# Kernel optimization log

Hardware: AMD Instinct MI355X
Metric: run time of the kernel (lower is better)

## Reference

```python
import jax, jax.numpy as jnp
import numpy as np
from jax import lax

IMG, P, C, D, H, L, B = 256, 16, 3, 768, 12, 8, 2
G = IMG // P            # 16
N = G * G               # 256 patches
FF = 2048               # hard-coded FFN hidden dim in ViTBlockWithCCAttention
DH = D // H
EPS = 1e-5


def setup_inputs() -> dict:
    key = jax.random.key(0)
    ks = jax.random.split(key, 24)
    s = 0.02
    rn = lambda k, shp: jax.random.normal(k, shp, jnp.float32) * s
    inp = {
        "x": jax.random.normal(ks[0], (B, C, IMG, IMG), jnp.float32),
        "patch_w": rn(ks[1], (D, C * P * P)),
        "patch_b": rn(ks[2], (D,)),
        "pos_embed": rn(ks[3], (1, N, D)),
        # per-layer stacked params (shared nn.MultiheadAttention per block)
        "in_proj_w": rn(ks[4], (L, 3 * D, D)),
        "in_proj_b": rn(ks[5], (L, 3 * D)),
        "out_w": rn(ks[6], (L, D, D)),
        "out_b": rn(ks[7], (L, D)),
        "ln1_g": jnp.ones((L, D), jnp.float32),
        "ln1_b": jnp.zeros((L, D), jnp.float32),
        "ln2_g": jnp.ones((L, D), jnp.float32),
        "ln2_b": jnp.zeros((L, D), jnp.float32),
        "ffn_w1": rn(ks[8], (L, FF, D)),
        "ffn_b1": rn(ks[9], (L, FF)),
        "ffn_w2": rn(ks[10], (L, D, FF)),
        "ffn_b2": rn(ks[11], (L, D)),
        "edge_w": rn(ks[12], (D, 1)),
        "edge_b": rn(ks[13], (D,)),
        "conv1_w": rn(ks[14], (256, D, 3, 3)),
        "conv1_b": rn(ks[15], (256,)),
        "conv2_w": rn(ks[16], (1, 256, 1, 1)),
        "conv2_b": rn(ks[17], (1,)),
    }
    return inp


def _ln(z, g, b):
    m = z.mean(-1, keepdims=True)
    v = ((z - m) ** 2).mean(-1, keepdims=True)
    return (z - m) / jnp.sqrt(v + EPS) * g + b


def _mha(z, wi, bi, wo, bo):
    # z: (M, S, D). Returns out (M,S,D) and head-averaged attn weights (M,S,S)
    M, S, _ = z.shape
    qkv = z @ wi.T + bi
    q, k, v = jnp.split(qkv, 3, axis=-1)
    sp = lambda t: t.reshape(M, S, H, DH).transpose(0, 2, 1, 3)  # (M,H,S,dh)
    q, k, v = sp(q), sp(k), sp(v)
    a = jax.nn.softmax(jnp.einsum('mhqd,mhkd->mhqk', q, k) / np.sqrt(DH).astype(np.float32), axis=-1)
    o = jnp.einsum('mhqk,mhkd->mhqd', a, v).transpose(0, 2, 1, 3).reshape(M, S, D)
    return o @ wo.T + bo, a.mean(1)


def reference(x, patch_w, patch_b, pos_embed, in_proj_w, in_proj_b, out_w, out_b,
              ln1_g, ln1_b, ln2_g, ln2_b, ffn_w1, ffn_b1, ffn_w2, ffn_b2,
              edge_w, edge_b, conv1_w, conv1_b, conv2_w, conv2_b):
    Bc = x.shape[0]
    # patch embedding: unfold -> (B, N, C*P*P) -> linear
    patches = x.reshape(Bc, C, G, P, G, P).transpose(0, 2, 4, 1, 3, 5).reshape(Bc, N, C * P * P)
    h = patches @ patch_w.T + patch_b + pos_embed

    edge_sum = jnp.zeros((Bc, N, D), h.dtype)
    for i in range(L):
        xl = _ln(h, ln1_g[i], ln1_b[i])
        x2d = xl.reshape(Bc, G, G, D)
        # rows: sequences along height, one per column
        row_x = x2d.transpose(0, 2, 1, 3).reshape(Bc * G, G, D)
        row_out, row_a = _mha(row_x, in_proj_w[i], in_proj_b[i], out_w[i], out_b[i])
        # cols: sequences along width, one per row
        col_x = x2d.reshape(Bc * G, G, D)
        col_out, col_a = _mha(col_x, in_proj_w[i], in_proj_b[i], out_w[i], out_b[i])
        attn_out = (row_out.reshape(Bc, G, G, D).transpose(0, 2, 1, 3)
                    + col_out.reshape(Bc, G, G, D)).reshape(Bc, N, D)
        h = h + attn_out
        z = _ln(h, ln2_g[i], ln2_b[i])
        h = h + jax.nn.relu(z @ ffn_w1[i].T + ffn_b1[i]) @ ffn_w2[i].T + ffn_b2[i]
        # attention-divergence edge tokens (query-averaged attn maps)
        div = jnp.abs(row_a.mean(1) - col_a.mean(1)).reshape(Bc, N, 1)
        edge_sum = edge_sum + (div @ edge_w.T + edge_b)
    h = h + edge_sum / L

    feat = h.transpose(0, 2, 1).reshape(Bc, D, G, G)
    feat = jax.image.resize(feat, (Bc, D, IMG, IMG), method="bilinear")  # align_corners=False
    dn = ("NCHW", "OIHW", "NCHW")
    y = lax.conv_general_dilated(feat, conv1_w, (1, 1), "SAME", dimension_numbers=dn)
    y = jax.nn.relu(y + conv1_b[None, :, None, None])
    y = lax.conv_general_dilated(y, conv2_w, (1, 1), "SAME", dimension_numbers=dn)
    return y + conv2_b[None, :, None, None]
```

## Files before the change

### kernel.cpp

```cpp
#include <hip/hip_runtime.h>
#include <hip/hip_bf16.h>
#include <math.h>

#define BB 2
#define CIN 3
#define IMGS 256
#define PS 16
#define GG 16
#define NN 256
#define DIM 768
#define NH 12
#define NL 8
#define FFD 2048
#define LNEPS 1e-5f

typedef __attribute__((ext_vector_type(8))) short bf16x8;
typedef __attribute__((ext_vector_type(8))) unsigned short u16x8;
typedef __attribute__((ext_vector_type(4))) unsigned short u16x4;
typedef __attribute__((ext_vector_type(4))) float f32x4;

#define MB     1
#define MB2    2
#define MPOS   4
#define MRELU  8
#define MRES   16
#define MOBF16 32
#define MAS2   64
#define MLNA   256
#define MAIM2  512
#define MSTATP 1024

#define IPW_N  1769472
#define OW_N   589824
#define F1_N   1572864
#define F2_N   1572864
#define WCT_N  1769472
#define PW_N   589824

__device__ inline unsigned short bc(float f) {
    return __builtin_bit_cast(unsigned short, __float2bfloat16(f));
}
__device__ inline float fbc(unsigned short u) {
    unsigned int x = ((unsigned int)u) << 16;
    return __builtin_bit_cast(float, x);
}

__device__ inline void gload16(const unsigned short* g, unsigned short* l) {
    __builtin_amdgcn_global_load_lds((const __attribute__((address_space(1))) void*)g,
                                     (__attribute__((address_space(3))) void*)l, 16, 0, 0);
}

template<int MODE, int BN>
__global__ __launch_bounds__(256) void gemm_bf16(
    const void* __restrict__ Av, const void* __restrict__ A2v,
    const unsigned short* __restrict__ B16,
    const float* __restrict__ bias, const float* __restrict__ pos,
    const float2* __restrict__ pstat,
    const float* __restrict__ lng, const float* __restrict__ lnb,
    float2* __restrict__ pstatOut,
    float* __restrict__ C, unsigned short* __restrict__ C16,
    int M, int N, int K, int zdiv,
    long long sAo, long long sBi, long long sCo, long long sCi)
{
    constexpr int NI = BN / 32;
    int z = blockIdx.y;
    int zo = z / zdiv, zi = z % zdiv;
    const unsigned short* A16 = (const unsigned short*)Av + (size_t)zo * sAo;
    const float* Af  = (const float*)Av  + (size_t)zo * sAo;
    const float* Af2 = (const float*)A2v + (size_t)zo * sAo;
    B16 += (size_t)zi * sBi;
    long long coff = (long long)zo * sCo + (long long)zi * sCi;

    int NBY = M >> 5;
    int nbysh = 31 - __builtin_clz(NBY);
    int id = blockIdx.x;
    int qch = gridDim.x >> 3;
    int wgid = (id & 7) * qch + (id >> 3);
    int bx = wgid >> nbysh, by = wgid & (NBY - 1);
    int bm = by * 32, bn = bx * BN;

    __shared__ __align__(16) unsigned short As[2][2048], Bs[2][BN * 64];
    __shared__ float2 sstat[32];
    int tid = threadIdx.x;
    int lane = tid & 63, wave = tid >> 6;
    int wr = wave >> 1, wc = wave & 1;
    int sA = tid;
    int srowA = sA >> 3, schkA = (sA & 7) ^ (srowA & 7);

    if constexpr (MODE & MLNA) {
        int row = tid >> 3, j = tid & 7;
        const float2* pr = pstat + (size_t)(bm + row) * 48 + j * 6;
        float s = 0.f, s2 = 0.f;
        #pragma unroll
        for (int k = 0; k < 6; ++k) { float2 v = pr[k]; s += v.x; s2 += v.y; }
        #pragma unroll
        for (int m2 = 1; m2 < 8; m2 <<= 1) {
            s  += __shfl_xor(s, m2);
            s2 += __shfl_xor(s2, m2);
        }
        if (j == 0) {
            float mean = s * (1.f / DIM);
            float var = s2 * (1.f / DIM) - mean * mean;
            sstat[row] = make_float2(mean, rsqrtf(var + LNEPS));
        }
        __syncthreads();
    }

    f32x4 acc[NI] = {};
    f32x4 rA0, rA1, rA20, rA21, gv0, gv1, bv0, bv1;
    float2 strow;

    auto gstageA = [&](int b, int kt) {
        gload16(A16 + (size_t)(bm + srowA) * K + kt * 64 + schkA * 8, &As[b][sA * 8]);
    };
    auto gstageB = [&](int b, int kt) {
        #pragma unroll
        for (int i = 0; i < NI; ++i) {
            int s = tid + i * 256;
            int row = s >> 3, chk = (s & 7) ^ (row & 7);
            gload16(B16 + (size_t)(bn + row) * K + kt * 64 + chk * 8, &Bs[b][s * 8]);
        }
    };
    auto ldA = [&](int kt) {
        int k0 = kt * 64 + schkA * 8;
        if constexpr (MODE & MAIM2) {
            int m = bm + srowA;
            int bq = m >> 8, n = m & 255, gy = n >> 4, gx = n & 15;
            int c = k0 >> 8, rem = k0 & 255, py = rem >> 4, px = rem & 15;
            const float* src = Af + (((size_t)(bq * CIN + c) * IMGS + gy * PS + py) << 8)
                             + gx * PS + px;
            rA0 = *(const f32x4*)(src);
            rA1 = *(const f32x4*)(src + 4);
        } else {
            size_t off = (size_t)(bm + srowA) * K + k0;
            rA0 = *(const f32x4*)(Af + off);
            rA1 = *(const f32x4*)(Af + off + 4);
            if constexpr (MODE & MAS2) {
                rA20 = *(const f32x4*)(Af2 + off);
                rA21 = *(const f32x4*)(Af2 + off + 4);
            }
            if constexpr (MODE & MLNA) {
                strow = sstat[srowA];
                gv0 = *(const f32x4*)(lng + k0); gv1 = *(const f32x4*)(lng + k0 + 4);
                bv0 = *(const f32x4*)(lnb + k0); bv1 = *(const f32x4*)(lnb + k0 + 4);
            }
        }
    };
    auto wrA = [&](int b) {
        bf16x8 v;
        #pragma unroll
        for (int j = 0; j < 4; ++j) {
            float x0 = rA0[j], x1 = rA1[j];
            if constexpr (MODE & MAS2) { x0 += rA20[j]; x1 += rA21[j]; }
            if constexpr (MODE & MLNA) {
                x0 = (x0 - strow.x) * strow.y * gv0[j] + bv0[j];
                x1 = (x1 - strow.x) * strow.y * gv1[j] + bv1[j];
            }
            v[j] = (short)bc(x0); v[4 + j] = (short)bc(x1);
        }
        *(bf16x8*)(&As[b][sA * 8]) = v;
    };
    constexpr bool regA = (MODE & (MAS2 | MLNA | MAIM2)) != 0;
    auto compute = [&](int b) {
        const unsigned short* Ab = As[b];
        const unsigned short* Bb = Bs[b];
        int rl = lane & 15, kh = lane >> 4;
        #pragma unroll
        for (int ks = 0; ks < 2; ++ks) {
            int kc = ks * 4 + kh;
            int ar = 16 * wr + rl;
            bf16x8 af = *(const bf16x8*)(Ab + ar * 64 + (kc ^ (ar & 7)) * 8);
            #pragma unroll
            for (int ni = 0; ni < NI; ++ni) {
                int br = 16 * NI * wc + 16 * ni + rl;
                bf16x8 bf = *(const bf16x8*)(Bb + br * 64 + (kc ^ (br & 7)) * 8);
                acc[ni] = __builtin_amdgcn_mfma_f32_16x16x32_bf16(af, bf, acc[ni], 0, 0, 0);
            }
        }
    };

    int nt = K >> 6;
    if constexpr (!regA) gstageA(0, 0); else { ldA(0); wrA(0); }
    gstageB(0, 0);
    __syncthreads();
    int buf = 0;
    for (int t = 0; t < nt; ++t) {
        if (t + 1 < nt) {
            if constexpr (!regA) gstageA(buf ^ 1, t + 1); else ldA(t + 1);
            gstageB(buf ^ 1, t + 1);
        }
        compute(buf);
        if (t + 1 < nt) {
            if constexpr (regA) wrA(buf ^ 1);
        }
        __syncthreads();
        buf ^= 1;
    }

    float vfin[4];
    #pragma unroll
    for (int ni = 0; ni < NI; ++ni) {
        #pragma unroll
        for (int r = 0; r < 4; ++r) {
            int row = bm + 16 * wr + (lane >> 4) * 4 + r;
            int col = bn + 16 * NI * wc + 16 * ni + (lane & 15);
            float v = acc[ni][r];
            if (MODE & (MB | MB2)) v += bias[col] * ((MODE & MB2) ? 2.f : 1.f);
            if (MODE & MPOS) v += pos[(size_t)(row & (NN - 1)) * N + col];
            if (MODE & MRELU) v = fmaxf(v, 0.f);
            long long ci = coff + (long long)row * N + col;
            if (MODE & MOBF16) { C16[ci] = bc(v); }
            else if (MODE & MRES) { v += C[ci]; C[ci] = v; }
            else { C[ci] = v; }
            if (ni == 0) vfin[r] = v;
        }
    }
    if constexpr (MODE & MSTATP) {
        #pragma unroll
        for (int r = 0; r < 4; ++r) {
            float s = vfin[r], s2 = vfin[r] * vfin[r];
            #pragma unroll
            for (int m2 = 1; m2 < 16; m2 <<= 1) {
                s  += __shfl_xor(s, m2);
                s2 += __shfl_xor(s2, m2);
            }
            if ((lane & 15) == 0) {
                int row = bm + 16 * wr + (lane >> 4) * 4 + r;
                pstatOut[(size_t)row * 48 + bx * 2 + wc] = make_float2(s, s2);
            }
        }
    }
}

__global__ __launch_bounds__(256) void wct_kernel(const float* __restrict__ conv1_w,
                                                  unsigned short* __restrict__ Wct16)
{
    int oc = blockIdx.x;
    int tid = threadIdx.x;
    __shared__ float w[6912];
    const float* src = conv1_w + (size_t)oc * 6912;
    #pragma unroll
    for (int k = 0; k < 27; ++k) w[tid + k * 256] = src[tid + k * 256];
    __syncthreads();
    #pragma unroll
    for (int dydx = 0; dydx < 9; ++dydx) {
        #pragma unroll
        for (int k = 0; k < 3; ++k) {
            int c = tid + k * 256;
            Wct16[(size_t)dydx * 196608 + oc * 768 + c] = bc(w[c * 9 + dydx]);
        }
    }
}

__global__ __launch_bounds__(256) void cvtflat_kernel(
    const float* __restrict__ ipw, const float* __restrict__ ow,
    const float* __restrict__ f1, const float* __restrict__ f2,
    const float* __restrict__ pw,
    unsigned short* __restrict__ d_ipw, unsigned short* __restrict__ d_ow,
    unsigned short* __restrict__ d_f1, unsigned short* __restrict__ d_f2,
    unsigned short* __restrict__ d_pw)
{
    int y = blockIdx.y;
    const float* src; unsigned short* dst; int n;
    if (y == 0)      { src = ipw; dst = d_ipw; n = 8 * IPW_N; }
    else if (y == 1) { src = ow;  dst = d_ow;  n = 8 * OW_N; }
    else if (y == 2) { src = f1;  dst = d_f1;  n = 8 * F1_N; }
    else if (y == 3) { src = f2;  dst = d_f2;  n = 8 * F2_N; }
    else             { src = pw;  dst = d_pw;  n = PW_N; }
    int base = blockIdx.x * 4096;
    if (base >= n) return;
    int t4 = threadIdx.x * 4;
    #pragma unroll
    for (int k = 0; k < 4; ++k) {
        int off = base + k * 1024 + t4;
        f32x4 v = *(const f32x4*)(src + off);
        u16x4 o;
        o[0] = bc(v[0]); o[1] = bc(v[1]); o[2] = bc(v[2]); o[3] = bc(v[3]);
        *(u16x4*)(dst + off) = o;
    }
}

__global__ __launch_bounds__(256) void attn_kernel(
    const float* __restrict__ qkv, float* __restrict__ orow,
    float* __restrict__ ocol, float* __restrict__ amh)
{
    int b = blockIdx.x >> 4, g = blockIdx.x & 15;
    int type = blockIdx.y;
    int hh = blockIdx.z;
    int tid = threadIdx.x;
    __shared__ float qs[16][68], ks[16][68], vs[16][68], as_[16][17];
    {
        int sr = tid >> 4, dq = tid & 15;
        int n = (type == 0) ? (sr * GG + g) : (g * GG + sr);
        const float* base = qkv + (size_t)(b * NN + n) * (3 * DIM) + hh * 64 + dq * 4;
        float4 qv = *(const float4*)(base);
        float4 kv = *(const float4*)(base + DIM);
        float4 vv = *(const float4*)(base + 2 * DIM);
        *(float4*)&qs[sr][dq * 4] = qv;
        *(float4*)&ks[sr][dq * 4] = kv;
        *(float4*)&vs[sr][dq * 4] = vv;
    }
    __syncthreads();
    int s = tid >> 4, t = tid & 15;
    float sc = 0.f;
    #pragma unroll
    for (int d = 0; d < 64; ++d) sc += qs[s][d] * ks[t][d];
    sc *= 0.125f;
    float mx = sc;
    #pragma unroll
    for (int off = 1; off < 16; off <<= 1) mx = fmaxf(mx, __shfl_xor(mx, off, 16));
    float p = __expf(sc - mx);
    float sum = p;
    #pragma unroll
    for (int off = 1; off < 16; off <<= 1) sum += __shfl_xor(sum, off, 16);
    as_[s][t] = p / sum;
    __syncthreads();
    if (tid < 16) {
        float a = 0.f;
        #pragma unroll
        for (int ss = 0; ss < 16; ++ss) a += as_[ss][tid];
        amh[((size_t)(type * BB + b) * NN + g * GG + tid) * NH + hh] = a;
    }
    int s2 = tid >> 4, dg = (tid & 15) * 4;
    float o0 = 0, o1 = 0, o2 = 0, o3 = 0;
    #pragma unroll
    for (int t2 = 0; t2 < 16; ++t2) {
        float a2 = as_[s2][t2];
        o0 += a2 * vs[t2][dg];
        o1 += a2 * vs[t2][dg + 1];
        o2 += a2 * vs[t2][dg + 2];
        o3 += a2 * vs[t2][dg + 3];
    }
    int n2 = (type == 0) ? (s2 * GG + g) : (g * GG + s2);
    float* op = ((type == 0) ? orow : ocol) + (size_t)(b * NN + n2) * DIM + hh * 64 + dg;
    *(float4*)op = make_float4(o0, o1, o2, o3);
}

__global__ __launch_bounds__(256) void hfin_kernel(
    const float* __restrict__ h, const float* __restrict__ amh,
    const float* __restrict__ ew, const float* __restrict__ eb,
    unsigned short* __restrict__ hf)
{
    int m = blockIdx.x;
    int b = m >> 8, n = m & 255;
    int tid = threadIdx.x;
    __shared__ float divs;
    if (tid < 8) {
        const float* base = amh + (size_t)tid * 12288 + (size_t)b * 3072 + n * 12;
        float rs = 0.f, cs = 0.f;
        #pragma unroll
        for (int hh = 0; hh < NH; ++hh) {
            rs += base[hh];
            cs += base[6144 + hh];
        }
        float d = fabsf(rs - cs);
        d += __shfl_xor(d, 1);
        d += __shfl_xor(d, 2);
        d += __shfl_xor(d, 4);
        if (tid == 0) divs = d * (1.f / (NH * GG)) * (1.f / NL);
    }
    __syncthreads();
    float dv = divs;
    const float* hp = h + (size_t)m * DIM;
    unsigned short* yp = hf + (size_t)m * DIM;
    #pragma unroll
    for (int seg = 0; seg < 3; ++seg) {
        int d0 = tid + seg * 256;
        yp[d0] = bc(hp[d0] + dv * ew[d0] + eb[d0]);
    }
}

__global__ __launch_bounds__(256) void s_kernel(const float* __restrict__ P,
                                               unsigned short* __restrict__ S16)
{
    int bdy = blockIdx.y;
    int b = bdy / 3, dy = bdy % 3;
    int ocg = blockIdx.x;
    __shared__ float Pl[3][4][16][17];
    int tid = threadIdx.x;
    #pragma unroll
    for (int l = 0; l < 12; ++l) {
        int e = l * 256 + tid;
        int dx = e >> 10, rem = e & 1023;
        int oc = rem >> 8, pix = rem & 255;
        int i = pix >> 4, j = pix & 15;
        Pl[dx][oc][j][i] =
            P[(((size_t)b * 9 + dy * 3 + dx) * 256 + ocg * 4 + oc) * 256 + pix];
    }
    __syncthreads();
    int xq = tid >> 6, oc = (tid >> 4) & 3, i = tid & 15;
    for (int xx = 0; xx < 64; ++xx) {
        int x = xq * 64 + xx;
        float acc = 0.f;
        #pragma unroll
        for (int dx = 0; dx < 3; ++dx) {
            int u = x + dx - 1;
            float p = (u + 0.5f) * 0.0625f - 0.5f;
            float fl = floorf(p);
            float f = p - fl;
            int j0 = (int)fl;
            int ja = j0 < 0 ? 0 : j0;
            int jb = (j0 + 1 > 15) ? 15 : (j0 + 1);
            bool valid = (u >= 0) && (u <= 255);
            float w0 = valid ? 1.f - f : 0.f;
            float w1 = valid ? f : 0.f;
            acc += w0 * Pl[dx][oc][ja][i] + w1 * Pl[dx][oc][jb][i];
        }
        S16[(((size_t)(b * 256 + x) * 3 + dy) * 256 + ocg * 4 + oc) * 16 + i] = bc(acc);
    }
}

__global__ __launch_bounds__(256) void out_kernel(
    const unsigned short* __restrict__ S16, const float* __restrict__ b1,
    const float* __restrict__ w2, const float* __restrict__ b2p,
    float* __restrict__ out)
{
    int b = blockIdx.x >> 8, x = blockIdx.x & 255;
    __shared__ float Sl[12288];
    const unsigned short* Sp = S16 + (size_t)(b * 256 + x) * 12288;
    #pragma unroll
    for (int c = 0; c < 6; ++c) {
        int l8 = (c * 256 + threadIdx.x) * 8;
        u16x8 v = *(const u16x8*)(Sp + l8);
        #pragma unroll
        for (int j = 0; j < 8; ++j) Sl[l8 + j] = fbc(v[j]);
    }
    __syncthreads();
    int y = threadIdx.x;
    float wy[3][2];
    int iy[3][2];
    #pragma unroll
    for (int dy = 0; dy < 3; ++dy) {
        int v = y + dy - 1;
        if (v < 0 || v > 255) {
            wy[dy][0] = wy[dy][1] = 0.f;
            iy[dy][0] = iy[dy][1] = 0;
        } else {
            float pp = (v + 0.5f) * 0.0625f - 0.5f;
            float fl = floorf(pp);
            float f = pp - fl;
            int i0 = (int)fl;
            iy[dy][0] = i0 < 0 ? 0 : i0;
            iy[dy][1] = (i0 + 1 > 15) ? 15 : (i0 + 1);
            wy[dy][0] = 1.f - f;
            wy[dy][1] = f;
        }
    }
    float acc = 0.f;
    for (int oc = 0; oc < 256; ++oc) {
        float sv = 0.f;
        #pragma unroll
        for (int dy = 0; dy < 3; ++dy)
            sv += wy[dy][0] * Sl[dy * 4096 + oc * 16 + iy[dy][0]]
                + wy[dy][1] * Sl[dy * 4096 + oc * 16 + iy[dy][1]];
        sv += b1[oc];
        acc += fmaxf(sv, 0.f) * w2[oc];
    }
    out[(size_t)b * 65536 + y * 256 + x] = acc + b2p[0];
}

extern "C" void kernel_launch(void* const* d_in, const int* in_sizes, int n_in,
                              void* d_out, int out_size, void* d_ws, size_t ws_size,
                              hipStream_t stream)
{
    const float* x         = (const float*)d_in[0];
    const float* patch_w   = (const float*)d_in[1];
    const float* patch_b   = (const float*)d_in[2];
    const float* pos_embed = (const float*)d_in[3];
    const float* in_proj_w = (const float*)d_in[4];
    const float* in_proj_b = (const float*)d_in[5];
    const float* out_w     = (const float*)d_in[6];
    const float* out_b     = (const float*)d_in[7];
    const float* ln1_g     = (const float*)d_in[8];
    const float* ln1_b     = (const float*)d_in[9];
    const float* ln2_g     = (const float*)d_in[10];
    const float* ln2_b     = (const float*)d_in[11];
    const float* ffn_w1    = (const float*)d_in[12];
    const float* ffn_b1    = (const float*)d_in[13];
    const float* ffn_w2    = (const float*)d_in[14];
    const float* ffn_b2    = (const float*)d_in[15];
    const float* edge_w    = (const float*)d_in[16];
    const float* edge_b    = (const float*)d_in[17];
    const float* conv1_w   = (const float*)d_in[18];
    const float* conv1_b   = (const float*)d_in[19];
    const float* conv2_w   = (const float*)d_in[20];
    const float* conv2_b   = (const float*)d_in[21];
    float* out = (float*)d_out;
    float* ws = (float*)d_ws;

    float* h      = ws;
    float* qkv    = h + 393216;
    float* orow   = qkv + 1179648;
    float* ocol   = orow + 393216;
    float* Pb     = ocol + 393216;
    float* amh    = Pb + 1179648;
    float2* pstat = (float2*)(amh + 98304);
    unsigned short* Sb16   = (unsigned short*)(amh + 98304 + 49152);
    unsigned short* hid16  = Sb16 + 6291456;
    unsigned short* hfin16 = hid16 + 1048576;
    unsigned short* Wct16  = hfin16 + 393216;
    unsigned short* pw16   = Wct16 + 1769472;
    unsigned short* ipw16  = pw16 + 589824;
    unsigned short* ow16   = ipw16 + 8 * IPW_N;
    unsigned short* f116   = ow16 + 8 * OW_N;
    unsigned short* f216   = f116 + 8 * F1_N;

    cvtflat_kernel<<<dim3(3456, 5), 256, 0, stream>>>(
        in_proj_w, out_w, ffn_w1, ffn_w2, patch_w,
        ipw16, ow16, f116, f216, pw16);
    wct_kernel<<<dim3(256), 256, 0, stream>>>(conv1_w, Wct16);

    gemm_bf16<MB | MPOS | MAIM2 | MSTATP, 32><<<dim3(24 * 16), 256, 0, stream>>>(
        x, nullptr, pw16, patch_b, pos_embed, nullptr, nullptr, nullptr, pstat,
        h, nullptr, 512, 768, 768, 1, 0, 0, 0, 0);

    for (int l = 0; l < NL; ++l) {
        gemm_bf16<MB | MLNA, 64><<<dim3(36 * 16), 256, 0, stream>>>(
            h, nullptr, ipw16 + (size_t)l * IPW_N, in_proj_b + (size_t)l * 2304, nullptr,
            pstat, ln1_g + l * DIM, ln1_b + l * DIM, nullptr, qkv, nullptr,
            512, 2304, 768, 1, 0, 0, 0, 0);
        attn_kernel<<<dim3(BB * GG, 2, NH), 256, 0, stream>>>(
            qkv, orow, ocol, amh + (size_t)l * 12288);
        gemm_bf16<MB2 | MRES | MAS2 | MSTATP, 32><<<dim3(24 * 16), 256, 0, stream>>>(
            orow, ocol, ow16 + (size_t)l * OW_N, out_b + (size_t)l * DIM, nullptr,
            nullptr, nullptr, nullptr, pstat, h, nullptr,
            512, 768, 768, 1, 0, 0, 0, 0);
        gemm_bf16<MB | MRELU | MOBF16 | MLNA, 64><<<dim3(32 * 16), 256, 0, stream>>>(
            h, nullptr, f116 + (size_t)l * F1_N, ffn_b1 + (size_t)l * FFD, nullptr,
            pstat, ln2_g + l * DIM, ln2_b + l * DIM, nullptr, nullptr, hid16,
            512, 2048, 768, 1, 0, 0, 0, 0);
        gemm_bf16<MB | MRES | MSTATP, 32><<<dim3(24 * 16), 256, 0, stream>>>(
            hid16, nullptr, f216 + (size_t)l * F2_N, ffn_b2 + (size_t)l * DIM, nullptr,
            nullptr, nullptr, nullptr, pstat, h, nullptr,
            512, 768, 2048, 1, 0, 0, 0, 0);
    }

    hfin_kernel<<<dim3(512), 256, 0, stream>>>(h, amh, edge_w, edge_b, hfin16);
    gemm_bf16<0, 32><<<dim3(8 * 8, 18), 256, 0, stream>>>(
        Wct16, nullptr, hfin16, nullptr, nullptr, nullptr, nullptr, nullptr, nullptr,
        Pb, nullptr, 256, 256, 768,
        2, 196608LL, 196608LL, 65536LL, 589824LL);
    s_kernel<<<dim3(64, 6), 256, 0, stream>>>(Pb, Sb16);
    out_kernel<<<dim3(512), 256, 0, stream>>>(Sb16, conv1_b, conv2_w, conv2_b, out);
}
```

Before: 604.8 us.

## Convert fp32 weights to bf16 inside GEMM loads, drop bulk conversion kernel

Removes the upfront kernel that converted all layer weights to bf16, which wrote and re-read copies of every weight tensor. The GEMMs now load fp32 weights straight into registers, convert them, and write the bf16 values to LDS, through the same register-staged path already used for A. This cuts one full pass over the weights (read fp32, write bf16). In exchange each GEMM reads twice the weight bytes from global memory, and the B tile goes through registers instead of asynchronous direct-to-LDS loads, which adds register pressure and reduces overlap.

```diff
diff --git a/kernel.cpp b/kernel.cpp
--- a/kernel.cpp
+++ b/kernel.cpp
@@ -16,7 +16,6 @@
 
 typedef __attribute__((ext_vector_type(8))) short bf16x8;
 typedef __attribute__((ext_vector_type(8))) unsigned short u16x8;
-typedef __attribute__((ext_vector_type(4))) unsigned short u16x4;
 typedef __attribute__((ext_vector_type(4))) float f32x4;
 
 #define MB     1
@@ -26,17 +25,11 @@
 #define MRES   16
 #define MOBF16 32
 #define MAS2   64
+#define MBF32  128
 #define MLNA   256
 #define MAIM2  512
 #define MSTATP 1024
 
-#define IPW_N  1769472
-#define OW_N   589824
-#define F1_N   1572864
-#define F2_N   1572864
-#define WCT_N  1769472
-#define PW_N   589824
-
 __device__ inline unsigned short bc(float f) {
     return __builtin_bit_cast(unsigned short, __float2bfloat16(f));
 }
@@ -53,7 +46,7 @@
 template<int MODE, int BN>
 __global__ __launch_bounds__(256) void gemm_bf16(
     const void* __restrict__ Av, const void* __restrict__ A2v,
-    const unsigned short* __restrict__ B16,
+    const void* __restrict__ Bv,
     const float* __restrict__ bias, const float* __restrict__ pos,
     const float2* __restrict__ pstat,
     const float* __restrict__ lng, const float* __restrict__ lnb,
@@ -68,7 +61,8 @@
     const unsigned short* A16 = (const unsigned short*)Av + (size_t)zo * sAo;
     const float* Af  = (const float*)Av  + (size_t)zo * sAo;
     const float* Af2 = (const float*)A2v + (size_t)zo * sAo;
-    B16 += (size_t)zi * sBi;
+    const unsigned short* B16 = (const unsigned short*)Bv + (size_t)zi * sBi;
+    const float* Bf = (const float*)Bv + (size_t)zi * sBi;
     long long coff = (long long)zo * sCo + (long long)zi * sCi;
 
     int NBY = M >> 5;
@@ -107,7 +101,7 @@
     }
 
     f32x4 acc[NI] = {};
-    f32x4 rA0, rA1, rA20, rA21, gv0, gv1, bv0, bv1;
+    f32x4 rA0, rA1, rA20, rA21, rB[NI][2], gv0, gv1, bv0, bv1;
     float2 strow;
 
     auto gstageA = [&](int b, int kt) {
@@ -146,6 +140,16 @@
             }
         }
     };
+    auto ldB = [&](int kt) {
+        #pragma unroll
+        for (int i = 0; i < NI; ++i) {
+            int s = tid + i * 256;
+            int row = s >> 3, chk = (s & 7) ^ (row & 7);
+            size_t off = (size_t)(bn + row) * K + kt * 64 + chk * 8;
+            rB[i][0] = *(const f32x4*)(Bf + off);
+            rB[i][1] = *(const f32x4*)(Bf + off + 4);
+        }
+    };
     auto wrA = [&](int b) {
         bf16x8 v;
         #pragma unroll
@@ -159,6 +163,18 @@
             v[j] = (short)bc(x0); v[4 + j] = (short)bc(x1);
         }
         *(bf16x8*)(&As[b][sA * 8]) = v;
+    };
+    auto wrB = [&](int b) {
+        #pragma unroll
+        for (int i = 0; i < NI; ++i) {
+            int s = tid + i * 256;
+            bf16x8 v;
+            #pragma unroll
+            for (int j = 0; j < 4; ++j) {
+                v[j] = (short)bc(rB[i][0][j]); v[4 + j] = (short)bc(rB[i][1][j]);
+            }
+            *(bf16x8*)(&Bs[b][s * 8]) = v;
+        }
     };
     constexpr bool regA = (MODE & (MAS2 | MLNA | MAIM2)) != 0;
     auto compute = [&](int b) {
@@ -181,17 +197,18 @@
 
     int nt = K >> 6;
     if constexpr (!regA) gstageA(0, 0); else { ldA(0); wrA(0); }
-    gstageB(0, 0);
+    if constexpr (!(MODE & MBF32)) gstageB(0, 0); else { ldB(0); wrB(0); }
     __syncthreads();
     int buf = 0;
     for (int t = 0; t < nt; ++t) {
         if (t + 1 < nt) {
             if constexpr (!regA) gstageA(buf ^ 1, t + 1); else ldA(t + 1);
-            gstageB(buf ^ 1, t + 1);
+            if constexpr (!(MODE & MBF32)) gstageB(buf ^ 1, t + 1); else ldB(t + 1);
         }
         compute(buf);
         if (t + 1 < nt) {
             if constexpr (regA) wrA(buf ^ 1);
+            if constexpr (MODE & MBF32) wrB(buf ^ 1);
         }
         __syncthreads();
         buf ^= 1;
@@ -249,34 +266,6 @@
             int c = tid + k * 256;
             Wct16[(size_t)dydx * 196608 + oc * 768 + c] = bc(w[c * 9 + dydx]);
         }
-    }
-}
-
-__global__ __launch_bounds__(256) void cvtflat_kernel(
-    const float* __restrict__ ipw, const float* __restrict__ ow,
-    const float* __restrict__ f1, const float* __restrict__ f2,
-    const float* __restrict__ pw,
-    unsigned short* __restrict__ d_ipw, unsigned short* __restrict__ d_ow,
-    unsigned short* __restrict__ d_f1, unsigned short* __restrict__ d_f2,
-    unsigned short* __restrict__ d_pw)
-{
-    int y = blockIdx.y;
-    const float* src; unsigned short* dst; int n;
-    if (y == 0)      { src = ipw; dst = d_ipw; n = 8 * IPW_N; }
-    else if (y == 1) { src = ow;  dst = d_ow;  n = 8 * OW_N; }
-    else if (y == 2) { src = f1;  dst = d_f1;  n = 8 * F1_N; }
-    else if (y == 3) { src = f2;  dst = d_f2;  n = 8 * F2_N; }
-    else             { src = pw;  dst = d_pw;  n = PW_N; }
-    int base = blockIdx.x * 4096;
-    if (base >= n) return;
-    int t4 = threadIdx.x * 4;
-    #pragma unroll
-    for (int k = 0; k < 4; ++k) {
-        int off = base + k * 1024 + t4;
-        f32x4 v = *(const f32x4*)(src + off);
-        u16x4 o;
-        o[0] = bc(v[0]); o[1] = bc(v[1]); o[2] = bc(v[2]); o[3] = bc(v[3]);
-        *(u16x4*)(dst + off) = o;
     }
 }
 
@@ -499,38 +488,34 @@
     unsigned short* hid16  = Sb16 + 6291456;
     unsigned short* hfin16 = hid16 + 1048576;
     unsigned short* Wct16  = hfin16 + 393216;
-    unsigned short* pw16   = Wct16 + 1769472;
-    unsigned short* ipw16  = pw16 + 589824;
-    unsigned short* ow16   = ipw16 + 8 * IPW_N;
-    unsigned short* f116   = ow16 + 8 * OW_N;
-    unsigned short* f216   = f116 + 8 * F1_N;
-
-    cvtflat_kernel<<<dim3(3456, 5), 256, 0, stream>>>(
-        in_proj_w, out_w, ffn_w1, ffn_w2, patch_w,
-        ipw16, ow16, f116, f216, pw16);
+
     wct_kernel<<<dim3(256), 256, 0, stream>>>(conv1_w, Wct16);
 
-    gemm_bf16<MB | MPOS | MAIM2 | MSTATP, 32><<<dim3(24 * 16), 256, 0, stream>>>(
-        x, nullptr, pw16, patch_b, pos_embed, nullptr, nullptr, nullptr, pstat,
+    gemm_bf16<MB | MPOS | MAIM2 | MBF32 | MSTATP, 32><<<dim3(24 * 16), 256, 0, stream>>>(
+        x, nullptr, patch_w, patch_b, pos_embed, nullptr, nullptr, nullptr, pstat,
         h, nullptr, 512, 768, 768, 1, 0, 0, 0, 0);
 
     for (int l = 0; l < NL; ++l) {
-        gemm_bf16<MB | MLNA, 64><<<dim3(36 * 16), 256, 0, stream>>>(
-            h, nullptr, ipw16 + (size_t)l * IPW_N, in_proj_b + (size_t)l * 2304, nullptr,
+        gemm_bf16<MB | MLNA | MBF32, 64><<<dim3(36 * 16), 256, 0, stream>>>(
+            h, nullptr, in_proj_w + (size_t)l * 1769472,
+            in_proj_b + (size_t)l * 2304, nullptr,
             pstat, ln1_g + l * DIM, ln1_b + l * DIM, nullptr, qkv, nullptr,
             512, 2304, 768, 1, 0, 0, 0, 0);
         attn_kernel<<<dim3(BB * GG, 2, NH), 256, 0, stream>>>(
             qkv, orow, ocol, amh + (size_t)l * 12288);
-        gemm_bf16<MB2 | MRES | MAS2 | MSTATP, 32><<<dim3(24 * 16), 256, 0, stream>>>(
-            orow, ocol, ow16 + (size_t)l * OW_N, out_b + (size_t)l * DIM, nullptr,
+        gemm_bf16<MB2 | MRES | MAS2 | MBF32 | MSTATP, 32><<<dim3(24 * 16), 256, 0, stream>>>(
+            orow, ocol, out_w + (size_t)l * 589824,
+            out_b + (size_t)l * DIM, nullptr,
             nullptr, nullptr, nullptr, pstat, h, nullptr,
             512, 768, 768, 1, 0, 0, 0, 0);
-        gemm_bf16<MB | MRELU | MOBF16 | MLNA, 64><<<dim3(32 * 16), 256, 0, stream>>>(
-            h, nullptr, f116 + (size_t)l * F1_N, ffn_b1 + (size_t)l * FFD, nullptr,
+        gemm_bf16<MB | MRELU | MOBF16 | MLNA | MBF32, 64><<<dim3(32 * 16), 256, 0, stream>>>(
+            h, nullptr, ffn_w1 + (size_t)l * 1572864,
+            ffn_b1 + (size_t)l * FFD, nullptr,
             pstat, ln2_g + l * DIM, ln2_b + l * DIM, nullptr, nullptr, hid16,
             512, 2048, 768, 1, 0, 0, 0, 0);
-        gemm_bf16<MB | MRES | MSTATP, 32><<<dim3(24 * 16), 256, 0, stream>>>(
-            hid16, nullptr, f216 + (size_t)l * F2_N, ffn_b2 + (size_t)l * DIM, nullptr,
+        gemm_bf16<MB | MRES | MBF32 | MSTATP, 32><<<dim3(24 * 16), 256, 0, stream>>>(
+            hid16, nullptr, ffn_w2 + (size_t)l * 1572864,
+            ffn_b2 + (size_t)l * DIM, nullptr,
             nullptr, nullptr, nullptr, pstat, h, nullptr,
             512, 768, 2048, 1, 0, 0, 0, 0);
     }
```

Result: faster. 592.9 us (median of 2 runs) (-2.0%).
